# Kernel optimization log

Measured on AMD Instinct MI355X. Metric: run time of the kernel, lower is better.

## Reference

```python
import jax, jax.numpy as jnp
import numpy as np

F_CH = 12   # self.f
R = 2       # self.r
LN_EPS = 1e-5


def setup_inputs() -> dict:
    key = jax.random.key(0)
    ks = jax.random.split(key, 12)
    B, C, h, w = 1024, 200, 15, 15
    f, fr = F_CH, F_CH // R
    X = jax.random.normal(ks[0], (B, C, h, w), dtype=jnp.float32)
    # 1x1 conv weights stored as [out, in]; biases [out]
    s_in = 1.0 / np.sqrt(C)
    w11 = jax.random.normal(ks[1], (f, C), dtype=jnp.float32) * s_in
    b11 = jax.random.normal(ks[2], (f,), dtype=jnp.float32) * 0.01
    w21 = jax.random.normal(ks[3], (f, C), dtype=jnp.float32) * s_in
    b21 = jax.random.normal(ks[4], (f,), dtype=jnp.float32) * 0.01
    w31 = jax.random.normal(ks[5], (f, C), dtype=jnp.float32) * s_in
    b31 = jax.random.normal(ks[6], (f,), dtype=jnp.float32) * 0.01
    w41 = jax.random.normal(ks[7], (fr, f), dtype=jnp.float32) * (1.0 / np.sqrt(f))
    b41 = jax.random.normal(ks[8], (fr,), dtype=jnp.float32) * 0.01
    w42 = jax.random.normal(ks[9], (C, fr), dtype=jnp.float32) * (1.0 / np.sqrt(fr))
    b42 = jax.random.normal(ks[10], (C,), dtype=jnp.float32) * 0.01
    ln_g = jnp.ones((C,), dtype=jnp.float32)
    ln_b = jnp.zeros((C,), dtype=jnp.float32)
    return {"X": X, "w11": w11, "b11": b11, "w21": w21, "b21": b21,
            "w31": w31, "b31": b31, "w41": w41, "b41": b41,
            "w42": w42, "b42": b42, "ln_g": ln_g, "ln_b": ln_b}


def reference(X, w11, b11, w21, b21, w31, b31, w41, b41, w42, b42, ln_g, ln_b):
    B, C, h, w = X.shape
    f = F_CH
    HW = h * w
    Xf = X.reshape(B, C, HW)                       # flatten spatial for 1x1 convs
    k = jnp.einsum('bcn,fc->bfn', Xf, w11) + b11[:, None]   # [B,f,HW]
    q = jnp.einsum('bcn,fc->bfn', Xf, w21) + b21[:, None]
    kq = k * q                                               # [B,f,HW]
    v = jnp.einsum('bcn,fc->bfn', Xf, w31) + b31[:, None]    # [B,f,HW]
    # original: permute to [B,h,w,f] then raw reshape to [B,f,1,HW] (scrambles data)
    vp = jnp.transpose(v.reshape(B, f, h, w), (0, 2, 3, 1)).reshape(B, f, HW)
    vm = jnp.mean(vp, axis=-1)                               # adaptive avg pool -> [B,f]
    vs = jax.nn.softmax(vm, axis=1)                          # nn.Softmax default dim=1 on 4D
    # einsum 'bkij,blik->bijl' with i=1: out[b,j,l] = (sum_k kq[b,k,j]) * vs[b,l]
    kqs = jnp.sum(kq, axis=1)                                # [B,HW]
    x41 = kqs[:, :, None] * vs[:, None, :]                   # [B,HW,f]
    x = x41 @ w41.T + b41                                    # conv41: [B,HW,f//r]
    x = x @ w42.T + b42                                      # conv42: [B,HW,C]
    mu = jnp.mean(x, axis=-1, keepdims=True)
    var = jnp.var(x, axis=-1, keepdims=True)
    xn = (x - mu) / jnp.sqrt(var + LN_EPS) * ln_g + ln_b     # LayerNorm(C)
    x42 = jax.nn.sigmoid(jax.nn.relu(xn))                    # [B,HW,C]
    gate = jnp.transpose(x42, (0, 2, 1)).reshape(B, C, h, w)
    return gate * X
```

## Files before the change

### kernel.cpp

```cpp
#include <hip/hip_runtime.h>
#include <math.h>

#define F_CH 12
#define C_DIM 200
#define HW 225
#define PERB (C_DIM*HW)
#define PERB4 (PERB/4)
#define LN_EPS 1e-5f

#define WS_WT   0
#define WS_DP   7200
#define WS_VARD 7400

__global__ __launch_bounds__(256) void k_prep(
    const float* __restrict__ w11, const float* __restrict__ w21,
    const float* __restrict__ w31, const float* __restrict__ b41,
    const float* __restrict__ w42, const float* __restrict__ b42,
    float* __restrict__ wT, float* __restrict__ Dp, float* __restrict__ varD)
{
    const int tid = threadIdx.x;
    for (int i = tid; i < 36*C_DIM; i += 256) {
        int c = i / 36, g = i - 36*c;
        float v;
        if (g < 12)      v = w11[g*C_DIM + c];
        else if (g < 24) v = w21[(g-12)*C_DIM + c];
        else             v = w31[(g-24)*C_DIM + c];
        wT[i] = v;
    }
    __shared__ float red[12];
    __shared__ float DmSh;
    float d = 0.f;
    if (tid < C_DIM) {
        float s = b42[tid];
#pragma unroll
        for (int j = 0; j < 6; ++j) s = fmaf(w42[tid*6+j], b41[j], s);
        d = s;
    }
    float s0 = d;
    for (int o = 32; o > 0; o >>= 1) s0 += __shfl_down(s0, o, 64);
    if ((tid & 63) == 0) red[tid >> 6] = s0;
    __syncthreads();
    if (tid == 0) DmSh = (red[0]+red[1]+red[2]+red[3]) * (1.f/C_DIM);
    __syncthreads();
    float dp = (tid < C_DIM) ? (d - DmSh) : 0.f;
    if (tid < C_DIM) Dp[tid] = dp;
    float s1 = dp*dp;
    for (int o = 32; o > 0; o >>= 1) s1 += __shfl_down(s1, o, 64);
    if ((tid & 63) == 0) red[4 + (tid >> 6)] = s1;
    __syncthreads();
    if (tid == 0) varD[0] = (red[4]+red[5]+red[6]+red[7]) * (1.f/C_DIM);
}

__global__ __launch_bounds__(256) void k_main(
    const float* __restrict__ X,
    const float* __restrict__ wT,
    const float* __restrict__ b11, const float* __restrict__ b21,
    const float* __restrict__ b31,
    const float* __restrict__ w41,
    const float* __restrict__ w42,
    const float* __restrict__ Dp, const float* __restrict__ varDp,
    const float* __restrict__ ln_g, const float* __restrict__ ln_b,
    float* __restrict__ out)
{
    const int b   = blockIdx.x;
    const int tid = threadIdx.x;

    __shared__ float kqsS[HW];
    __shared__ float vmb[F_CH];
    __shared__ float vsS[F_CH];
    __shared__ float t1S[6];
    __shared__ float red[12];
    __shared__ float AmSh, varASh, covSh;
    __shared__ float AgS[C_DIM], DgS[C_DIM], blS[C_DIM];
    __shared__ float PS[HW], RS[HW];

    const float varD = varDp[0];

    float accK[F_CH], accQ[F_CH], accV[F_CH];
#pragma unroll
    for (int f = 0; f < F_CH; ++f) { accK[f] = b11[f]; accQ[f] = b21[f]; accV[f] = b31[f]; }

    const int n = (tid < HW) ? tid : (HW-1);
    const float* xcol = X + (size_t)b*PERB + n;
    for (int c = 0; c < C_DIM; ++c) {
        float x = xcol[c*HW];
        const float* wr = wT + c*36;
#pragma unroll
        for (int f = 0; f < F_CH; ++f) {
            accK[f] = fmaf(x, wr[f],      accK[f]);
            accQ[f] = fmaf(x, wr[12+f],   accQ[f]);
            accV[f] = fmaf(x, wr[24+f],   accV[f]);
        }
    }

    if (tid < F_CH) vmb[tid] = 0.f;
    if (tid < HW) {
        float s = 0.f;
#pragma unroll
        for (int f = 0; f < F_CH; ++f) s = fmaf(accK[f], accQ[f], s);
        kqsS[tid] = s;
    }
    __syncthreads();

    if (tid < HW) {
        int m0 = 12*tid;
        int a0 = m0/225, a1 = (m0+11)/225;
        if (a0 == a1) {
            float s = 0.f;
#pragma unroll
            for (int f = 0; f < F_CH; ++f) s += accV[f];
            atomicAdd(&vmb[a0], s);
        } else {
            int split = 225*a1 - m0;
            float sa = 0.f, sb = 0.f;
#pragma unroll
            for (int f = 0; f < F_CH; ++f) { if (f < split) sa += accV[f]; else sb += accV[f]; }
            atomicAdd(&vmb[a0], sa);
            atomicAdd(&vmb[a1], sb);
        }
    }
    __syncthreads();

    if (tid == 0) {
        float v[F_CH], mx = -1e30f;
#pragma unroll
        for (int a = 0; a < F_CH; ++a) { v[a] = vmb[a]*(1.f/HW); mx = fmaxf(mx, v[a]); }
        float s = 0.f;
#pragma unroll
        for (int a = 0; a < F_CH; ++a) { v[a] = __expf(v[a]-mx); s += v[a]; }
        float inv = 1.f/s;
#pragma unroll
        for (int a = 0; a < F_CH; ++a) vsS[a] = v[a]*inv;
    }
    __syncthreads();

    if (tid < 6) {
        float s = 0.f;
#pragma unroll
        for (int l = 0; l < F_CH; ++l) s = fmaf(w41[tid*F_CH+l], vsS[l], s);
        t1S[tid] = s;
    }
    __syncthreads();

    float A = 0.f, AD = 0.f;
    if (tid < C_DIM) {
        float s = 0.f;
#pragma unroll
        for (int j = 0; j < 6; ++j) s = fmaf(w42[tid*6+j], t1S[j], s);
        A = s;
        AD = A * Dp[tid];
    }
    float r0 = A, r1 = A*A, r2 = AD;
    for (int o = 32; o > 0; o >>= 1) {
        r0 += __shfl_down(r0, o, 64);
        r1 += __shfl_down(r1, o, 64);
        r2 += __shfl_down(r2, o, 64);
    }
    if ((tid & 63) == 0) { int w = tid>>6; red[w*3]=r0; red[w*3+1]=r1; red[w*3+2]=r2; }
    __syncthreads();
    if (tid == 0) {
        float S0 = red[0]+red[3]+red[6]+red[9];
        float S1 = red[1]+red[4]+red[7]+red[10];
        float S2 = red[2]+red[5]+red[8]+red[11];
        float Am = S0*(1.f/C_DIM);
        AmSh   = Am;
        varASh = S1*(1.f/C_DIM) - Am*Am;
        covSh  = S2*(1.f/C_DIM);
    }
    __syncthreads();

    if (tid < C_DIM) {
        float Ap = A - AmSh;
        float g  = ln_g[tid];
        AgS[tid] = Ap*g;
        DgS[tid] = Dp[tid]*g;
        blS[tid] = ln_b[tid];
    }
    if (tid < HW) {
        float kq  = kqsS[tid];
        float var = fmaf(kq*kq, varASh, fmaf(2.f*kq, covSh, varD));
        float rs  = rsqrtf(var + LN_EPS);
        PS[tid] = kq*rs;
        RS[tid] = rs;
    }
    __syncthreads();

    const float4* __restrict__ X4 = (const float4*)(X + (size_t)b*PERB);
    float4* __restrict__ O4 = (float4*)(out + (size_t)b*PERB);
    for (int i = tid; i < PERB4; i += 256) {
        float4 xv = X4[i];
        float xs[4] = {xv.x, xv.y, xv.z, xv.w};
        float rs4[4];
        unsigned base = (unsigned)i*4u;
#pragma unroll
        for (int e = 0; e < 4; ++e) {
            unsigned idx = base + e;
            unsigned c  = idx / HW;
            unsigned nn = idx - c*HW;
            float xn = fmaf(PS[nn], AgS[c], fmaf(RS[nn], DgS[c], blS[c]));
            float gate = (xn > 0.f) ? (1.f/(1.f+__expf(-xn))) : 0.5f;
            rs4[e] = gate * xs[e];
        }
        float4 ov; ov.x=rs4[0]; ov.y=rs4[1]; ov.z=rs4[2]; ov.w=rs4[3];
        O4[i] = ov;
    }
}

extern "C" void kernel_launch(void* const* d_in, const int* in_sizes, int n_in,
                              void* d_out, int out_size, void* d_ws, size_t ws_size,
                              hipStream_t stream) {
    const float* X   = (const float*)d_in[0];
    const float* w11 = (const float*)d_in[1];
    const float* b11 = (const float*)d_in[2];
    const float* w21 = (const float*)d_in[3];
    const float* b21 = (const float*)d_in[4];
    const float* w31 = (const float*)d_in[5];
    const float* b31 = (const float*)d_in[6];
    const float* w41 = (const float*)d_in[7];
    const float* b41 = (const float*)d_in[8];
    const float* w42 = (const float*)d_in[9];
    const float* b42 = (const float*)d_in[10];
    const float* lng = (const float*)d_in[11];
    const float* lnb = (const float*)d_in[12];
    float* out = (float*)d_out;
    float* ws  = (float*)d_ws;

    float* wT = ws + WS_WT;
    float* Dp = ws + WS_DP;
    float* vD = ws + WS_VARD;

    hipLaunchKernelGGL(k_prep, dim3(1), dim3(256), 0, stream,
                       w11, w21, w31, b41, w42, b42, wT, Dp, vD);
    hipLaunchKernelGGL(k_main, dim3(1024), dim3(256), 0, stream,
                       X, wT, b11, b21, b31, w41, w42, Dp, vD, lng, lnb, out);
}
```

Before: 401.4 us.

## Split main kernel into register-tiled projection and chunked gate-apply kernels

The fused kernel is split into two. k_gemm gives each wave 9 output channels times 4 spatial positions per lane, loading X as float4, and stages the results in shared memory before the kq and v reductions. k_apply precomputes the sigmoid gate for 40-channel chunks into shared memory, then multiplies X by it with float4 loads and stores. This raises FMA reuse per load and separates the transcendental work from streaming, at the cost of a third launch, a second full read of X, and a workspace round-trip for the per-batch LayerNorm factors.

```diff
diff --git a/kernel.cpp b/kernel.cpp
--- a/kernel.cpp
+++ b/kernel.cpp
@@ -5,12 +5,13 @@
 #define C_DIM 200
 #define HW 225
 #define PERB (C_DIM*HW)
-#define PERB4 (PERB/4)
 #define LN_EPS 1e-5f
 
 #define WS_WT   0
 #define WS_DP   7200
 #define WS_VARD 7400
+#define WS_PB   7424
+#define PB_STRIDE 896
 
 __global__ __launch_bounds__(256) void k_prep(
     const float* __restrict__ w11, const float* __restrict__ w21,
@@ -51,70 +52,119 @@
     if (tid == 0) varD[0] = (red[4]+red[5]+red[6]+red[7]) * (1.f/C_DIM);
 }
 
-__global__ __launch_bounds__(256) void k_main(
-    const float* __restrict__ X,
-    const float* __restrict__ wT,
+__global__ __launch_bounds__(256) void k_gemm(
+    const float* __restrict__ X, const float* __restrict__ wT,
     const float* __restrict__ b11, const float* __restrict__ b21,
     const float* __restrict__ b31,
-    const float* __restrict__ w41,
-    const float* __restrict__ w42,
+    const float* __restrict__ w41, const float* __restrict__ w42,
     const float* __restrict__ Dp, const float* __restrict__ varDp,
     const float* __restrict__ ln_g, const float* __restrict__ ln_b,
-    float* __restrict__ out)
+    float* __restrict__ ws)
 {
-    const int b   = blockIdx.x;
-    const int tid = threadIdx.x;
-
+    const int b    = blockIdx.x;
+    const int tid  = threadIdx.x;
+    const int lane = tid & 63;
+    const int f0   = 9 * (int)__builtin_amdgcn_readfirstlane((unsigned)(threadIdx.x >> 6));
+
+    __shared__ float accS[36][228];
     __shared__ float kqsS[HW];
     __shared__ float vmb[F_CH];
     __shared__ float vsS[F_CH];
     __shared__ float t1S[6];
     __shared__ float red[12];
     __shared__ float AmSh, varASh, covSh;
-    __shared__ float AgS[C_DIM], DgS[C_DIM], blS[C_DIM];
-    __shared__ float PS[HW], RS[HW];
-
-    const float varD = varDp[0];
-
-    float accK[F_CH], accQ[F_CH], accV[F_CH];
-#pragma unroll
-    for (int f = 0; f < F_CH; ++f) { accK[f] = b11[f]; accQ[f] = b21[f]; accV[f] = b31[f]; }
-
-    const int n = (tid < HW) ? tid : (HW-1);
-    const float* xcol = X + (size_t)b*PERB + n;
-    for (int c = 0; c < C_DIM; ++c) {
-        float x = xcol[c*HW];
-        const float* wr = wT + c*36;
+
+    const float* __restrict__ xb = X + (size_t)b * PERB;
+    const bool vec = (lane < 56);
+    const int  p0  = vec ? 4*lane : 224;
+
+    float acc[9][4];
+#pragma unroll
+    for (int j = 0; j < 9; ++j)
+#pragma unroll
+        for (int e = 0; e < 4; ++e) acc[j][e] = 0.f;
+
+    for (int cb = 0; cb < C_DIM; cb += 4) {
+        float4 x0, x1, x2, x3;
+        if (vec) {
+            x0 = *(const float4*)(xb + (cb+0)*HW + p0);
+            x1 = *(const float4*)(xb + (cb+1)*HW + p0);
+            x2 = *(const float4*)(xb + (cb+2)*HW + p0);
+            x3 = *(const float4*)(xb + (cb+3)*HW + p0);
+        } else {
+            float s0 = xb[(cb+0)*HW + 224];
+            float s1 = xb[(cb+1)*HW + 224];
+            float s2 = xb[(cb+2)*HW + 224];
+            float s3 = xb[(cb+3)*HW + 224];
+            x0 = make_float4(s0,s0,s0,s0);
+            x1 = make_float4(s1,s1,s1,s1);
+            x2 = make_float4(s2,s2,s2,s2);
+            x3 = make_float4(s3,s3,s3,s3);
+        }
+        const float* wr0 = wT + (cb+0)*36 + f0;
+        const float* wr1 = wT + (cb+1)*36 + f0;
+        const float* wr2 = wT + (cb+2)*36 + f0;
+        const float* wr3 = wT + (cb+3)*36 + f0;
+#pragma unroll
+        for (int j = 0; j < 9; ++j) {
+            float w0 = wr0[j], w1 = wr1[j], w2 = wr2[j], w3 = wr3[j];
+            acc[j][0] = fmaf(w0, x0.x, acc[j][0]);
+            acc[j][1] = fmaf(w0, x0.y, acc[j][1]);
+            acc[j][2] = fmaf(w0, x0.z, acc[j][2]);
+            acc[j][3] = fmaf(w0, x0.w, acc[j][3]);
+            acc[j][0] = fmaf(w1, x1.x, acc[j][0]);
+            acc[j][1] = fmaf(w1, x1.y, acc[j][1]);
+            acc[j][2] = fmaf(w1, x1.z, acc[j][2]);
+            acc[j][3] = fmaf(w1, x1.w, acc[j][3]);
+            acc[j][0] = fmaf(w2, x2.x, acc[j][0]);
+            acc[j][1] = fmaf(w2, x2.y, acc[j][1]);
+            acc[j][2] = fmaf(w2, x2.z, acc[j][2]);
+            acc[j][3] = fmaf(w2, x2.w, acc[j][3]);
+            acc[j][0] = fmaf(w3, x3.x, acc[j][0]);
+            acc[j][1] = fmaf(w3, x3.y, acc[j][1]);
+            acc[j][2] = fmaf(w3, x3.z, acc[j][2]);
+            acc[j][3] = fmaf(w3, x3.w, acc[j][3]);
+        }
+    }
+
+    if (vec) {
+#pragma unroll
+        for (int j = 0; j < 9; ++j) {
+            float4 v = make_float4(acc[j][0], acc[j][1], acc[j][2], acc[j][3]);
+            *(float4*)&accS[f0 + j][p0] = v;
+        }
+    } else if (lane == 56) {
+#pragma unroll
+        for (int j = 0; j < 9; ++j) accS[f0 + j][224] = acc[j][0];
+    }
+    if (tid < F_CH) vmb[tid] = 0.f;
+    __syncthreads();
+
+    if (tid < HW) {
+        float kq = 0.f;
 #pragma unroll
         for (int f = 0; f < F_CH; ++f) {
-            accK[f] = fmaf(x, wr[f],      accK[f]);
-            accQ[f] = fmaf(x, wr[12+f],   accQ[f]);
-            accV[f] = fmaf(x, wr[24+f],   accV[f]);
-        }
-    }
-
-    if (tid < F_CH) vmb[tid] = 0.f;
-    if (tid < HW) {
-        float s = 0.f;
-#pragma unroll
-        for (int f = 0; f < F_CH; ++f) s = fmaf(accK[f], accQ[f], s);
-        kqsS[tid] = s;
-    }
-    __syncthreads();
-
-    if (tid < HW) {
+            float kf = accS[f][tid]      + b11[f];
+            float qf = accS[12+f][tid]   + b21[f];
+            kq = fmaf(kf, qf, kq);
+        }
+        kqsS[tid] = kq;
+
+        float vf[F_CH];
+#pragma unroll
+        for (int f = 0; f < F_CH; ++f) vf[f] = accS[24+f][tid] + b31[f];
         int m0 = 12*tid;
         int a0 = m0/225, a1 = (m0+11)/225;
         if (a0 == a1) {
             float s = 0.f;
 #pragma unroll
-            for (int f = 0; f < F_CH; ++f) s += accV[f];
+            for (int f = 0; f < F_CH; ++f) s += vf[f];
             atomicAdd(&vmb[a0], s);
         } else {
             int split = 225*a1 - m0;
             float sa = 0.f, sb = 0.f;
 #pragma unroll
-            for (int f = 0; f < F_CH; ++f) { if (f < split) sa += accV[f]; else sb += accV[f]; }
+            for (int f = 0; f < F_CH; ++f) { if (f < split) sa += vf[f]; else sb += vf[f]; }
             atomicAdd(&vmb[a0], sa);
             atomicAdd(&vmb[a1], sb);
         }
@@ -128,7 +178,7 @@
         float s = 0.f;
 #pragma unroll
         for (int a = 0; a < F_CH; ++a) { v[a] = __expf(v[a]-mx); s += v[a]; }
-        float inv = 1.f/s;
+        float inv = __builtin_amdgcn_rcpf(s);
 #pragma unroll
         for (int a = 0; a < F_CH; ++a) vsS[a] = v[a]*inv;
     }
@@ -169,40 +219,67 @@
     }
     __syncthreads();
 
+    float* __restrict__ wsb = ws + WS_PB + (size_t)b * PB_STRIDE;
     if (tid < C_DIM) {
-        float Ap = A - AmSh;
-        float g  = ln_g[tid];
-        AgS[tid] = Ap*g;
-        DgS[tid] = Dp[tid]*g;
-        blS[tid] = ln_b[tid];
+        float g = ln_g[tid];
+        wsb[450 + tid] = (A - AmSh) * g;
+        wsb[650 + tid] = Dp[tid] * g;
     }
     if (tid < HW) {
         float kq  = kqsS[tid];
-        float var = fmaf(kq*kq, varASh, fmaf(2.f*kq, covSh, varD));
-        float rs  = rsqrtf(var + LN_EPS);
-        PS[tid] = kq*rs;
-        RS[tid] = rs;
-    }
-    __syncthreads();
-
-    const float4* __restrict__ X4 = (const float4*)(X + (size_t)b*PERB);
-    float4* __restrict__ O4 = (float4*)(out + (size_t)b*PERB);
-    for (int i = tid; i < PERB4; i += 256) {
-        float4 xv = X4[i];
-        float xs[4] = {xv.x, xv.y, xv.z, xv.w};
-        float rs4[4];
-        unsigned base = (unsigned)i*4u;
-#pragma unroll
-        for (int e = 0; e < 4; ++e) {
-            unsigned idx = base + e;
-            unsigned c  = idx / HW;
-            unsigned nn = idx - c*HW;
-            float xn = fmaf(PS[nn], AgS[c], fmaf(RS[nn], DgS[c], blS[c]));
-            float gate = (xn > 0.f) ? (1.f/(1.f+__expf(-xn))) : 0.5f;
-            rs4[e] = gate * xs[e];
-        }
-        float4 ov; ov.x=rs4[0]; ov.y=rs4[1]; ov.z=rs4[2]; ov.w=rs4[3];
-        O4[i] = ov;
+        float var = fmaf(kq*kq, varASh, fmaf(2.f*kq, covSh, varDp[0]));
+        float rs  = __builtin_amdgcn_rsqf(var + LN_EPS);
+        wsb[tid]       = kq * rs;
+        wsb[225 + tid] = rs;
+    }
+}
+
+__global__ __launch_bounds__(256) void k_apply(
+    const float* __restrict__ X, const float* __restrict__ ws,
+    const float* __restrict__ ln_b, float* __restrict__ out)
+{
+    const int b   = blockIdx.x;
+    const int tid = threadIdx.x;
+
+    __shared__ float gS[9000];
+    __shared__ float PSs[HW], RSs[HW];
+    __shared__ float AgS[C_DIM], DgS[C_DIM], blS[C_DIM];
+
+    const float* __restrict__ wsb = ws + WS_PB + (size_t)b * PB_STRIDE;
+    if (tid < HW)    { PSs[tid] = wsb[tid]; RSs[tid] = wsb[225+tid]; }
+    if (tid < C_DIM) { AgS[tid] = wsb[450+tid]; DgS[tid] = wsb[650+tid]; blS[tid] = ln_b[tid]; }
+    __syncthreads();
+
+    const float* __restrict__ xb = X + (size_t)b * PERB;
+    float* __restrict__ ob = out + (size_t)b * PERB;
+
+    for (int chunk = 0; chunk < 5; ++chunk) {
+        const int c0   = chunk * 40;
+        const int base = chunk * 9000;
+        for (unsigned i = tid; i < 9000u; i += 256u) {
+            unsigned cl = i / 225u;
+            unsigned nn = i - 225u*cl;
+            unsigned c  = c0 + cl;
+            float xn = fmaf(PSs[nn], AgS[c], fmaf(RSs[nn], DgS[c], blS[c]));
+            float t  = fmaxf(xn, 0.f);
+            float g  = __builtin_amdgcn_rcpf(1.f + __expf(-t));
+            gS[i] = g;
+        }
+        __syncthreads();
+        const float4* __restrict__ X4 = (const float4*)(xb + base);
+        float4* __restrict__ O4 = (float4*)(ob + base);
+        const float4* __restrict__ G4 = (const float4*)gS;
+        for (unsigned i = tid; i < 2250u; i += 256u) {
+            float4 xv = X4[i];
+            float4 gv = G4[i];
+            float4 ov;
+            ov.x = xv.x * gv.x;
+            ov.y = xv.y * gv.y;
+            ov.z = xv.z * gv.z;
+            ov.w = xv.w * gv.w;
+            O4[i] = ov;
+        }
+        __syncthreads();
     }
 }
 
@@ -225,12 +302,12 @@
     float* out = (float*)d_out;
     float* ws  = (float*)d_ws;
 
-    float* wT = ws + WS_WT;
-    float* Dp = ws + WS_DP;
-    float* vD = ws + WS_VARD;
-
     hipLaunchKernelGGL(k_prep, dim3(1), dim3(256), 0, stream,
-                       w11, w21, w31, b41, w42, b42, wT, Dp, vD);
-    hipLaunchKernelGGL(k_main, dim3(1024), dim3(256), 0, stream,
-                       X, wT, b11, b21, b31, w41, w42, Dp, vD, lng, lnb, out);
+                       w11, w21, w31, b41, w42, b42,
+                       ws + WS_WT, ws + WS_DP, ws + WS_VARD);
+    hipLaunchKernelGGL(k_gemm, dim3(1024), dim3(256), 0, stream,
+                       X, ws + WS_WT, b11, b21, b31, w41, w42,
+                       ws + WS_DP, ws + WS_VARD, lng, lnb, ws);
+    hipLaunchKernelGGL(k_apply, dim3(1024), dim3(256), 0, stream,
+                       X, ws, lnb, out);
 }
```

Result: slower. 419.9 us (+4.6%).
